# Optimization experiments

Measured on AMD Instinct MI355X. Metric: run time of the kernel, lower is better.

Reference implementation:

```python
import jax, jax.numpy as jnp
import numpy as np

B, H, W, C = 8, 64, 64, 256
C8 = C // 8  # query/key channels


def setup_inputs() -> dict:
    key = jax.random.key(0)
    ks = jax.random.split(key, 8)
    s = 0.02  # init scale for weights
    return {
        "x": jax.random.normal(ks[0], (B, H, W, C), dtype=jnp.float32),
        "Wq": jax.random.normal(ks[1], (C, C8), dtype=jnp.float32) * s,
        "bq": jnp.zeros((C8,), dtype=jnp.float32),
        "Wk": jax.random.normal(ks[2], (C, C8), dtype=jnp.float32) * s,
        "bk": jnp.zeros((C8,), dtype=jnp.float32),
        "Wv": jax.random.normal(ks[3], (C, C), dtype=jnp.float32) * s,
        "bv": jnp.zeros((C,), dtype=jnp.float32),
        "gamma": jnp.full((1,), 0.5, dtype=jnp.float32),
    }


def reference(x, Wq, bq, Wk, bk, Wv, bv, gamma):
    Bn, Hn, Wn, Cn = x.shape
    N = Hn * Wn
    xf = x.reshape(Bn, N, Cn)            # flatten spatial dims: [B, N, C]
    # 1x1 convs == per-pixel dense projections over channels
    q = xf @ Wq + bq                     # [B, N, C//8]
    k = xf @ Wk + bk                     # [B, N, C//8]
    v = xf @ Wv + bv                     # [B, N, C]
    # energy[b,i,j] = k_i . q_j  (matches tf.matmul(key, query, transpose_b=True))
    energy = jnp.einsum('bic,bjc->bij', k, q)   # [B, N, N]
    attn = jax.nn.softmax(energy, axis=-1)      # softmax over last axis
    # out_i = sum_j attn[i,j] * v_j  (intended SAGAN aggregation in NHWC layout)
    out = jnp.einsum('bij,bjc->bic', attn, v)   # [B, N, C]
    out = out.reshape(Bn, Hn, Wn, Cn)
    return gamma * out + x
```

## Files before the change

kernel.cpp:

```cpp
#include <hip/hip_runtime.h>

typedef __attribute__((ext_vector_type(8))) short short8;
typedef __attribute__((ext_vector_type(4))) float f32x4;
typedef __attribute__((ext_vector_type(16))) float f32x16;
typedef __attribute__((ext_vector_type(2))) unsigned int u32x2;
typedef __attribute__((ext_vector_type(4))) unsigned int u32x4;
typedef unsigned short u16;
typedef unsigned int u32;

#define MFMA16(a, b, c) __builtin_amdgcn_mfma_f32_16x16x32_bf16((a), (b), (c), 0, 0, 0)
#define MFMA32(a, b, c) __builtin_amdgcn_mfma_f32_32x32x16_bf16((a), (b), (c), 0, 0, 0)

#define BATCH 8
#define NTOK 4096
#define CDIM 256
#define CQK 32
#define LOG2E 1.4426950408889634f

__device__ __forceinline__ u16 f2bf(float f) {
  u32 u = __float_as_uint(f);
  return (u16)((u + 0x7FFFu + ((u >> 16) & 1u)) >> 16);
}
__device__ __forceinline__ u32 pack2(float a, float b) {
  const u32 ua = __float_as_uint(a) + 0x8000u;
  const u32 ub = __float_as_uint(b) + 0x8000u;
#if __has_builtin(__builtin_amdgcn_perm)
  return __builtin_amdgcn_perm(ub, ua, 0x07060302u);
#else
  return (ua >> 16) | (ub & 0xFFFF0000u);
#endif
}
__device__ __forceinline__ float fexp2(float x) {
#if __has_builtin(__builtin_amdgcn_exp2f)
  return __builtin_amdgcn_exp2f(x);
#else
  return exp2f(x);
#endif
}

__global__ void k_prep(const float* __restrict__ Wq, const float* __restrict__ bq,
                       const float* __restrict__ Wk, const float* __restrict__ bk,
                       const float* __restrict__ Wv, const float* __restrict__ bv,
                       u16* __restrict__ wtf, float* __restrict__ bias) {
  const int f = blockIdx.x;
  const int L = threadIdx.x;
  const int ct = f >> 3, ks = f & 7;
  const int o = ct * 16 + (L & 15);
  const int ch = ks * 32 + (L >> 4) * 8;
  short8 v8;
#pragma unroll
  for (int jj = 0; jj < 8; jj++) {
    const int c = ch + jj;
    float v;
    if (o < 32)       v = Wq[c * CQK + o];
    else if (o < 64)  v = Wk[c * CQK + (o - 32)];
    else              v = Wv[c * CDIM + (o - 64)];
    v8[jj] = (short)f2bf(v);
  }
  *(short8*)(wtf + (size_t)f * 512 + L * 8) = v8;
  if (f == 0) {
    for (int i = L; i < 320; i += 64) {
      if (i < 32)      bias[i] = bq[i];
      else if (i < 64) bias[i] = bk[i - 32];
      else             bias[i] = bv[i - 64];
    }
  }
}

__global__ __launch_bounds__(256, 2) void k_proj(
    const float* __restrict__ x, const u16* __restrict__ wtf,
    const float* __restrict__ bias,
    u16* __restrict__ q_ws, u16* __restrict__ k_ws, u16* __restrict__ vt_ws) {
  __shared__ u16 x_lds[64 * 264];
  __shared__ u16 vt_t[64 * 76];
  const int m0 = blockIdx.x * 64;
  const int tid = threadIdx.x;
  const int w = tid >> 6, L = tid & 63;
  const int lr = L & 15, q4 = L >> 4;

  short8 wfA[5], wfB[5];
#pragma unroll
  for (int j = 0; j < 5; j++)
    wfA[j] = *(const short8*)(wtf + ((size_t)((j * 4 + w) * 8 + 0)) * 512 + L * 8);

#pragma unroll
  for (int ii = 0; ii < 8; ii++) {
    const int e = (tid + 256 * ii) * 8;
    const int row = e >> 8, col = e & 255;
    const float* src = x + (size_t)(m0 + row) * CDIM + col;
    f32x4 a = *(const f32x4*)src;
    f32x4 b4 = *(const f32x4*)(src + 4);
    u32x4 pk;
    pk[0] = pack2(a[0], a[1]);
    pk[1] = pack2(a[2], a[3]);
    pk[2] = pack2(b4[0], b4[1]);
    pk[3] = pack2(b4[2], b4[3]);
    *(u32x4*)&x_lds[row * 264 + col] = pk;
  }
  __syncthreads();

  f32x4 acc[4][5];
#pragma unroll
  for (int rg = 0; rg < 4; rg++)
#pragma unroll
    for (int j = 0; j < 5; j++) acc[rg][j] = (f32x4){0.f, 0.f, 0.f, 0.f};

#pragma unroll
  for (int ks = 0; ks < 8; ks++) {
    if (ks < 7) {
#pragma unroll
      for (int j = 0; j < 5; j++) {
        short8 v = *(const short8*)(wtf +
            ((size_t)((j * 4 + w) * 8 + ks + 1)) * 512 + L * 8);
        if (ks & 1) wfA[j] = v; else wfB[j] = v;
      }
    }
#pragma unroll
    for (int rg = 0; rg < 4; rg++) {
      short8 a = *(const short8*)&x_lds[(rg * 16 + lr) * 264 + ks * 32 + q4 * 8];
#pragma unroll
      for (int j = 0; j < 5; j++)
        acc[rg][j] = MFMA16(a, (ks & 1) ? wfB[j] : wfA[j], acc[rg][j]);
    }
  }

  {
    const float bb = bias[w * 16 + lr];
#pragma unroll
    for (int rg = 0; rg < 4; rg++)
#pragma unroll
      for (int r = 0; r < 4; r++) {
        const int row = m0 + rg * 16 + q4 * 4 + r;
        float v = acc[rg][0][r] + bb;
        if (w < 2) q_ws[(size_t)row * CQK + w * 16 + lr] = f2bf(v);
        else       k_ws[(size_t)row * CQK + (w - 2) * 16 + lr] = f2bf(v * LOG2E);
      }
  }
  const int b = m0 >> 12, nt = (m0 & 4095) >> 6;
  const int c_l = w * 16 + lr;
#pragma unroll
  for (int cg = 0; cg < 4; cg++) {
    __syncthreads();
    const int j = cg + 1;
    const float bb = bias[(4 + cg * 4 + w) * 16 + lr];
#pragma unroll
    for (int rg = 0; rg < 4; rg++) {
      u32x2 pk;
      pk[0] = pack2(acc[rg][j][0] + bb, acc[rg][j][1] + bb);
      pk[1] = pack2(acc[rg][j][2] + bb, acc[rg][j][3] + bb);
      *(u32x2*)&vt_t[c_l * 76 + rg * 16 + q4 * 4] = pk;
    }
    __syncthreads();
#pragma unroll
    for (int i = 0; i < 2; i++) {
      const int gch = tid + 256 * i;
      const int fid = gch >> 6;
      const int lane = gch & 63;
      const int jt = fid >> 2, kh = (fid >> 1) & 1, ct2 = fid & 1;
      const int cc = ct2 * 32 + (lane & 31);
      const int n0 = jt * 32 + kh * 16 + (lane >> 5) * 4;
      u32x2 va = *(const u32x2*)&vt_t[cc * 76 + n0];
      u32x2 vb2 = *(const u32x2*)&vt_t[cc * 76 + n0 + 8];
      u32x4 vv = {va[0], va[1], vb2[0], vb2[1]};
      *(short8*)(vt_ws +
          ((((size_t)(b * 64 + nt) * 4 + cg) * 8 + fid) * 512) + lane * 8) =
          __builtin_bit_cast(short8, vv);
    }
  }
}

__global__ __launch_bounds__(256, 2) void k_attn(
    const float* __restrict__ x, const u16* __restrict__ q_ws,
    const u16* __restrict__ k_ws, const u16* __restrict__ vt_ws,
    const float* __restrict__ gamma, float* __restrict__ out) {
  __shared__ float lp4[4][32];

  const int bid = blockIdx.x;
  const int b = bid & 7;
  const int tid = threadIdx.x;
  const int w = tid >> 6, L = tid & 63;
  const int L31 = L & 31, Lhi = L >> 5;
  const int i0 = (bid >> 3) * 64 + (w >> 1) * 32;
  const int chh = w & 1;

  const u16* kb = k_ws + ((size_t)(b * NTOK + i0 + L31)) * CQK + Lhi * 8;
  const short8 kf0 = *(const short8*)(kb);
  const short8 kf1 = *(const short8*)(kb + 16);
  const u16* qb = q_ws + ((size_t)(b * NTOK) + L31) * CQK + Lhi * 8;
  const u16* vb = vt_ws + ((size_t)b << 20) + (size_t)(chh * 2) * 4096 +
                  (size_t)L * 8;

  f32x16 z16;
#pragma unroll
  for (int e = 0; e < 16; e++) z16[e] = 0.f;
  f32x16 o00 = z16, o01 = z16, o10 = z16, o11 = z16;
  float ls = 0.f;

  short8 u0 = *(const short8*)(vb + 0);
  short8 u1 = *(const short8*)(vb + 512);
  short8 u2 = *(const short8*)(vb + 1024);
  short8 u3 = *(const short8*)(vb + 1536);
  short8 u4 = *(const short8*)(vb + 4096);
  short8 u5 = *(const short8*)(vb + 4096 + 512);
  short8 u6 = *(const short8*)(vb + 4096 + 1024);
  short8 u7 = *(const short8*)(vb + 4096 + 1536);
  short8 v0 = *(const short8*)(vb + 2048);
  short8 v1 = *(const short8*)(vb + 2048 + 512);
  short8 v2 = *(const short8*)(vb + 2048 + 1024);
  short8 v3 = *(const short8*)(vb + 2048 + 1536);
  short8 v4 = *(const short8*)(vb + 4096 + 2048);
  short8 v5 = *(const short8*)(vb + 4096 + 2048 + 512);
  short8 v6 = *(const short8*)(vb + 4096 + 2048 + 1024);
  short8 v7 = *(const short8*)(vb + 4096 + 2048 + 1536);
  short8 q00 = *(const short8*)(qb);
  short8 q01 = *(const short8*)(qb + 16);
  short8 q10 = *(const short8*)(qb + 32 * CQK);
  short8 q11 = *(const short8*)(qb + 32 * CQK + 16);

#define EPPV(SV, W0, W1, W2, W3, W4, W5, W6, W7)                               \
  do {                                                                         \
    float e0 = fexp2((SV)[0]), e1 = fexp2((SV)[1]);                            \
    float e2 = fexp2((SV)[2]), e3 = fexp2((SV)[3]);                            \
    float e4 = fexp2((SV)[4]), e5 = fexp2((SV)[5]);                            \
    float e6 = fexp2((SV)[6]), e7 = fexp2((SV)[7]);                            \
    float e8 = fexp2((SV)[8]), e9 = fexp2((SV)[9]);                            \
    float e10 = fexp2((SV)[10]), e11 = fexp2((SV)[11]);                        \
    float e12 = fexp2((SV)[12]), e13 = fexp2((SV)[13]);                        \
    float e14 = fexp2((SV)[14]), e15 = fexp2((SV)[15]);                        \
    ls += ((((e0 + e1) + (e2 + e3)) + ((e4 + e5) + (e6 + e7))) +               \
           (((e8 + e9) + (e10 + e11)) + ((e12 + e13) + (e14 + e15))));         \
    u32x4 pA = {pack2(e0, e1), pack2(e2, e3), pack2(e4, e5), pack2(e6, e7)};   \
    u32x4 pB = {pack2(e8, e9), pack2(e10, e11), pack2(e12, e13),               \
                pack2(e14, e15)};                                              \
    const short8 a0 = __builtin_bit_cast(short8, pA);                          \
    const short8 a1 = __builtin_bit_cast(short8, pB);                          \
    o00 = MFMA32(a0, W0, o00);                                                 \
    o01 = MFMA32(a0, W1, o01);                                                 \
    o10 = MFMA32(a0, W4, o10);                                                 \
    o11 = MFMA32(a0, W5, o11);                                                 \
    o00 = MFMA32(a1, W2, o00);                                                 \
    o01 = MFMA32(a1, W3, o01);                                                 \
    o10 = MFMA32(a1, W6, o10);                                                 \
    o11 = MFMA32(a1, W7, o11);                                                 \
  } while (0)

  for (int t = 0; t < 64; ++t) {
    const u16* vn = vb + (size_t)(t + 1) * 16384;
    f32x16 sv0 = MFMA32(q00, kf0, z16);
    sv0 = MFMA32(q01, kf1, sv0);
    EPPV(sv0, u0, u1, u2, u3, u4, u5, u6, u7);
    u0 = *(const short8*)(vn + 0);
    u1 = *(const short8*)(vn + 512);
    u2 = *(const short8*)(vn + 1024);
    u3 = *(const short8*)(vn + 1536);
    u4 = *(const short8*)(vn + 4096);
    u5 = *(const short8*)(vn + 4096 + 512);
    u6 = *(const short8*)(vn + 4096 + 1024);
    u7 = *(const short8*)(vn + 4096 + 1536);
    f32x16 sv1 = MFMA32(q10, kf0, z16);
    sv1 = MFMA32(q11, kf1, sv1);
    {
      const size_t qo = (size_t)(t + 1) * 64 * CQK;
      q00 = *(const short8*)(qb + qo);
      q01 = *(const short8*)(qb + qo + 16);
      q10 = *(const short8*)(qb + qo + 32 * CQK);
      q11 = *(const short8*)(qb + qo + 32 * CQK + 16);
    }
    EPPV(sv1, v0, v1, v2, v3, v4, v5, v6, v7);
    v0 = *(const short8*)(vn + 2048);
    v1 = *(const short8*)(vn + 2048 + 512);
    v2 = *(const short8*)(vn + 2048 + 1024);
    v3 = *(const short8*)(vn + 2048 + 1536);
    v4 = *(const short8*)(vn + 4096 + 2048);
    v5 = *(const short8*)(vn + 4096 + 2048 + 512);
    v6 = *(const short8*)(vn + 4096 + 2048 + 1024);
    v7 = *(const short8*)(vn + 4096 + 2048 + 1536);
  }
#undef EPPV

  ls += __shfl_xor(ls, 32);
  if (L < 32) lp4[w][L] = 1.0f / ls;
  asm volatile("s_waitcnt lgkmcnt(0)" ::: "memory");

  float linv[16];
#pragma unroll
  for (int rg = 0; rg < 16; rg++)
    linv[rg] = lp4[w][(rg & 3) + 8 * (rg >> 2) + 4 * Lhi];

  const float g = gamma[0];
#define STO(OV, CB2, CT2)                                                      \
  _Pragma("unroll")                                                            \
  for (int rg = 0; rg < 16; rg++) {                                            \
    const int i = i0 + (rg & 3) + 8 * (rg >> 2) + 4 * Lhi;                     \
    const int c = (chh * 2 + (CB2)) * 64 + (CT2) * 32 + L31;                   \
    const size_t idx = ((size_t)(b * NTOK + i)) * CDIM + c;                    \
    out[idx] = g * (OV[rg] * linv[rg]) + x[idx];                               \
  }
  STO(o00, 0, 0)
  STO(o01, 0, 1)
  STO(o10, 1, 0)
  STO(o11, 1, 1)
#undef STO
}

extern "C" void kernel_launch(void* const* d_in, const int* in_sizes, int n_in,
                              void* d_out, int out_size, void* d_ws, size_t ws_size,
                              hipStream_t stream) {
  const float* x  = (const float*)d_in[0];
  const float* Wq = (const float*)d_in[1];
  const float* bq = (const float*)d_in[2];
  const float* Wk = (const float*)d_in[3];
  const float* bk = (const float*)d_in[4];
  const float* Wv = (const float*)d_in[5];
  const float* bv = (const float*)d_in[6];
  const float* gamma = (const float*)d_in[7];
  float* out = (float*)d_out;

  char* ws = (char*)d_ws;
  u16* q_ws  = (u16*)(ws);
  u16* k_ws  = (u16*)(ws + (2u << 20));
  u16* vt_ws = (u16*)(ws + (4u << 20));
  u16* wtf   = (u16*)(ws + (20u << 20));
  float* bias = (float*)(ws + (20u << 20) + (256u << 10));

  k_prep<<<160, 64, 0, stream>>>(Wq, bq, Wk, bk, Wv, bv, wtf, bias);
  k_proj<<<512, 256, 0, stream>>>(x, wtf, bias, q_ws, k_ws, vt_ws);
  k_attn<<<512, 256, 0, stream>>>(x, q_ws, k_ws, vt_ws, gamma, out);
}
```

Baseline: 205.6 us.

## Split attention key dimension across warps and reduce partial outputs in LDS

Each block now covers 32 query rows instead of 64. Its four warps split the key sequence into two halves, and the upper two warps write their partial outputs and row sums to shared memory so the lower two can add them up and write the result. The grid doubles to 1024 blocks, the launch bounds ask for 4 blocks per CU, and V-fragment prefetching is restructured to hold only 8 registers, interleaved with the MFMAs. The aim is more parallelism and occupancy with lower register pressure. The cost is a shared-memory reduction, a block-wide barrier, and Q/K fragments loaded redundantly across the extra blocks.

New measurement: 256.1 us. 24.6% more time.

```diff
diff --git a/kernel.cpp b/kernel.cpp
--- a/kernel.cpp
+++ b/kernel.cpp
@@ -169,19 +169,23 @@
   }
 }
 
-__global__ __launch_bounds__(256, 2) void k_attn(
+__global__ __launch_bounds__(256, 4) void k_attn(
     const float* __restrict__ x, const u16* __restrict__ q_ws,
     const u16* __restrict__ k_ws, const u16* __restrict__ vt_ws,
     const float* __restrict__ gamma, float* __restrict__ out) {
-  __shared__ float lp4[4][32];
+  __shared__ float obuf[2][64][65];
+  __shared__ float rbuf[2][32];
+  __shared__ float lp2[2][32];
 
   const int bid = blockIdx.x;
   const int b = bid & 7;
+  const int i0 = (bid >> 3) * 32;
   const int tid = threadIdx.x;
   const int w = tid >> 6, L = tid & 63;
   const int L31 = L & 31, Lhi = L >> 5;
-  const int i0 = (bid >> 3) * 64 + (w >> 1) * 32;
   const int chh = w & 1;
+  const int jsel = w >> 1;
+  const int t0 = jsel * 32;
 
   const u16* kb = k_ws + ((size_t)(b * NTOK + i0 + L31)) * CQK + Lhi * 8;
   const short8 kf0 = *(const short8*)(kb);
@@ -196,28 +200,20 @@
   f32x16 o00 = z16, o01 = z16, o10 = z16, o11 = z16;
   float ls = 0.f;
 
-  short8 u0 = *(const short8*)(vb + 0);
-  short8 u1 = *(const short8*)(vb + 512);
-  short8 u2 = *(const short8*)(vb + 1024);
-  short8 u3 = *(const short8*)(vb + 1536);
-  short8 u4 = *(const short8*)(vb + 4096);
-  short8 u5 = *(const short8*)(vb + 4096 + 512);
-  short8 u6 = *(const short8*)(vb + 4096 + 1024);
-  short8 u7 = *(const short8*)(vb + 4096 + 1536);
-  short8 v0 = *(const short8*)(vb + 2048);
-  short8 v1 = *(const short8*)(vb + 2048 + 512);
-  short8 v2 = *(const short8*)(vb + 2048 + 1024);
-  short8 v3 = *(const short8*)(vb + 2048 + 1536);
-  short8 v4 = *(const short8*)(vb + 4096 + 2048);
-  short8 v5 = *(const short8*)(vb + 4096 + 2048 + 512);
-  short8 v6 = *(const short8*)(vb + 4096 + 2048 + 1024);
-  short8 v7 = *(const short8*)(vb + 4096 + 2048 + 1536);
-  short8 q00 = *(const short8*)(qb);
-  short8 q01 = *(const short8*)(qb + 16);
-  short8 q10 = *(const short8*)(qb + 32 * CQK);
-  short8 q11 = *(const short8*)(qb + 32 * CQK + 16);
-
-#define EPPV(SV, W0, W1, W2, W3, W4, W5, W6, W7)                               \
+  short8 u0 = *(const short8*)(vb + (size_t)t0 * 16384 + 0);
+  short8 u1 = *(const short8*)(vb + (size_t)t0 * 16384 + 512);
+  short8 u2 = *(const short8*)(vb + (size_t)t0 * 16384 + 1024);
+  short8 u3 = *(const short8*)(vb + (size_t)t0 * 16384 + 1536);
+  short8 u4 = *(const short8*)(vb + (size_t)t0 * 16384 + 4096);
+  short8 u5 = *(const short8*)(vb + (size_t)t0 * 16384 + 4096 + 512);
+  short8 u6 = *(const short8*)(vb + (size_t)t0 * 16384 + 4096 + 1024);
+  short8 u7 = *(const short8*)(vb + (size_t)t0 * 16384 + 4096 + 1536);
+  short8 q00 = *(const short8*)(qb + (size_t)t0 * 64 * CQK);
+  short8 q01 = *(const short8*)(qb + (size_t)t0 * 64 * CQK + 16);
+  short8 q10 = *(const short8*)(qb + (size_t)t0 * 64 * CQK + 32 * CQK);
+  short8 q11 = *(const short8*)(qb + (size_t)t0 * 64 * CQK + 32 * CQK + 16);
+
+#define EPPV(SV, NB)                                                           \
   do {                                                                         \
     float e0 = fexp2((SV)[0]), e1 = fexp2((SV)[1]);                            \
     float e2 = fexp2((SV)[2]), e3 = fexp2((SV)[3]);                            \
@@ -234,29 +230,29 @@
                 pack2(e14, e15)};                                              \
     const short8 a0 = __builtin_bit_cast(short8, pA);                          \
     const short8 a1 = __builtin_bit_cast(short8, pB);                          \
-    o00 = MFMA32(a0, W0, o00);                                                 \
-    o01 = MFMA32(a0, W1, o01);                                                 \
-    o10 = MFMA32(a0, W4, o10);                                                 \
-    o11 = MFMA32(a0, W5, o11);                                                 \
-    o00 = MFMA32(a1, W2, o00);                                                 \
-    o01 = MFMA32(a1, W3, o01);                                                 \
-    o10 = MFMA32(a1, W6, o10);                                                 \
-    o11 = MFMA32(a1, W7, o11);                                                 \
+    o00 = MFMA32(a0, u0, o00);                                                 \
+    o01 = MFMA32(a0, u1, o01);                                                 \
+    o10 = MFMA32(a0, u4, o10);                                                 \
+    o11 = MFMA32(a0, u5, o11);                                                 \
+    u0 = *(const short8*)((NB) + 0);                                           \
+    u1 = *(const short8*)((NB) + 512);                                         \
+    u4 = *(const short8*)((NB) + 4096);                                        \
+    u5 = *(const short8*)((NB) + 4096 + 512);                                  \
+    o00 = MFMA32(a1, u2, o00);                                                 \
+    o01 = MFMA32(a1, u3, o01);                                                 \
+    o10 = MFMA32(a1, u6, o10);                                                 \
+    o11 = MFMA32(a1, u7, o11);                                                 \
+    u2 = *(const short8*)((NB) + 1024);                                        \
+    u3 = *(const short8*)((NB) + 1536);                                        \
+    u6 = *(const short8*)((NB) + 4096 + 1024);                                 \
+    u7 = *(const short8*)((NB) + 4096 + 1536);                                 \
   } while (0)
 
-  for (int t = 0; t < 64; ++t) {
-    const u16* vn = vb + (size_t)(t + 1) * 16384;
+  for (int t = t0; t < t0 + 32; ++t) {
+    const u16* tb = vb + (size_t)t * 16384;
     f32x16 sv0 = MFMA32(q00, kf0, z16);
     sv0 = MFMA32(q01, kf1, sv0);
-    EPPV(sv0, u0, u1, u2, u3, u4, u5, u6, u7);
-    u0 = *(const short8*)(vn + 0);
-    u1 = *(const short8*)(vn + 512);
-    u2 = *(const short8*)(vn + 1024);
-    u3 = *(const short8*)(vn + 1536);
-    u4 = *(const short8*)(vn + 4096);
-    u5 = *(const short8*)(vn + 4096 + 512);
-    u6 = *(const short8*)(vn + 4096 + 1024);
-    u7 = *(const short8*)(vn + 4096 + 1536);
+    EPPV(sv0, tb + 2048);
     f32x16 sv1 = MFMA32(q10, kf0, z16);
     sv1 = MFMA32(q11, kf1, sv1);
     {
@@ -266,41 +262,55 @@
       q10 = *(const short8*)(qb + qo + 32 * CQK);
       q11 = *(const short8*)(qb + qo + 32 * CQK + 16);
     }
-    EPPV(sv1, v0, v1, v2, v3, v4, v5, v6, v7);
-    v0 = *(const short8*)(vn + 2048);
-    v1 = *(const short8*)(vn + 2048 + 512);
-    v2 = *(const short8*)(vn + 2048 + 1024);
-    v3 = *(const short8*)(vn + 2048 + 1536);
-    v4 = *(const short8*)(vn + 4096 + 2048);
-    v5 = *(const short8*)(vn + 4096 + 2048 + 512);
-    v6 = *(const short8*)(vn + 4096 + 2048 + 1024);
-    v7 = *(const short8*)(vn + 4096 + 2048 + 1536);
+    EPPV(sv1, tb + 16384);
   }
 #undef EPPV
 
   ls += __shfl_xor(ls, 32);
-  if (L < 32) lp4[w][L] = 1.0f / ls;
-  asm volatile("s_waitcnt lgkmcnt(0)" ::: "memory");
-
-  float linv[16];
-#pragma unroll
-  for (int rg = 0; rg < 16; rg++)
-    linv[rg] = lp4[w][(rg & 3) + 8 * (rg >> 2) + 4 * Lhi];
-
-  const float g = gamma[0];
+
+  if (w >= 2) {
+#pragma unroll
+    for (int e = 0; e < 16; e++) {
+      obuf[w - 2][L][e] = o00[e];
+      obuf[w - 2][L][16 + e] = o01[e];
+      obuf[w - 2][L][32 + e] = o10[e];
+      obuf[w - 2][L][48 + e] = o11[e];
+    }
+    if (L < 32) rbuf[w - 2][L] = ls;
+  }
+  __syncthreads();
+  if (w < 2) {
+#pragma unroll
+    for (int e = 0; e < 16; e++) {
+      o00[e] += obuf[w][L][e];
+      o01[e] += obuf[w][L][16 + e];
+      o10[e] += obuf[w][L][32 + e];
+      o11[e] += obuf[w][L][48 + e];
+    }
+    const float lst = ls + rbuf[w][L31];
+    if (L < 32) lp2[w][L] = 1.0f / lst;
+    asm volatile("s_waitcnt lgkmcnt(0)" ::: "memory");
+
+    float linv[16];
+#pragma unroll
+    for (int rg = 0; rg < 16; rg++)
+      linv[rg] = lp2[w][(rg & 3) + 8 * (rg >> 2) + 4 * Lhi];
+
+    const float g = gamma[0];
 #define STO(OV, CB2, CT2)                                                      \
   _Pragma("unroll")                                                            \
   for (int rg = 0; rg < 16; rg++) {                                            \
     const int i = i0 + (rg & 3) + 8 * (rg >> 2) + 4 * Lhi;                     \
-    const int c = (chh * 2 + (CB2)) * 64 + (CT2) * 32 + L31;                   \
+    const int c = (w * 2 + (CB2)) * 64 + (CT2) * 32 + L31;                     \
     const size_t idx = ((size_t)(b * NTOK + i)) * CDIM + c;                    \
     out[idx] = g * (OV[rg] * linv[rg]) + x[idx];                               \
   }
-  STO(o00, 0, 0)
-  STO(o01, 0, 1)
-  STO(o10, 1, 0)
-  STO(o11, 1, 1)
+    STO(o00, 0, 0)
+    STO(o01, 0, 1)
+    STO(o10, 1, 0)
+    STO(o11, 1, 1)
 #undef STO
+  }
 }
 
 extern "C" void kernel_launch(void* const* d_in, const int* in_sizes, int n_in,
@@ -325,5 +335,5 @@
 
   k_prep<<<160, 64, 0, stream>>>(Wq, bq, Wk, bk, Wv, bv, wtf, bias);
   k_proj<<<512, 256, 0, stream>>>(x, wtf, bias, q_ws, k_ws, vt_ws);
-  k_attn<<<512, 256, 0, stream>>>(x, q_ws, k_ws, vt_ws, gamma, out);
-}
+  k_attn<<<1024, 256, 0, stream>>>(x, q_ws, k_ws, vt_ws, gamma, out);
+}
```
